# Kernel optimization log

Measured on AMD Instinct MI355X. Metric: run time of the kernel, lower is better.

## Reference

```python
import jax, jax.numpy as jnp
import numpy as np

HIDDEN = 64
ALPHA = 0.2  # leaky relu negative slope
NEG_INF = -9e15


def setup_inputs() -> dict:
    key = jax.random.key(0)
    k1, k2, k3, k4, k5 = jax.random.split(key, 5)
    b, N, Fin, Fout = 8, 2048, 512, 256
    inp = jax.random.normal(k1, (b, N, Fin), dtype=jnp.float32)
    adj = jax.random.randint(k2, (b, N, N), 0, 2, dtype=jnp.int32)
    # xavier_uniform with gain=1.414 ~ uniform(-lim, lim)
    def xavier(k, shape):
        lim = 1.414 * np.sqrt(6.0 / (shape[0] + shape[1]))
        return jax.random.uniform(k, shape, jnp.float32, -lim, lim)
    weight = xavier(k3, (Fin, Fout))
    ht = xavier(k4, (Fout, HIDDEN))
    a = xavier(k5, (2 * HIDDEN, 1))
    return {"input": inp, "adj": adj, "weight": weight, "ht": ht, "a": a}


def reference(input, adj, weight, ht, a):
    # h: [b, N, Fout]
    h = jnp.matmul(input, weight)
    # trans_h: [b, N, HIDDEN]
    trans_h = jnp.einsum('bnc,ck->bnk', h, ht)
    # The original cat([th_i, th_j]) @ a decomposes as th_i@a1 + th_j@a2
    a1, a2 = a[:HIDDEN, 0], a[HIDDEN:, 0]
    f1 = trans_h @ a1  # [b, N] source (row) term
    f2 = trans_h @ a2  # [b, N] target (col) term
    e = f1[:, :, None] + f2[:, None, :]  # [b, N, N]
    e = jnp.where(e >= 0, e, ALPHA * e)  # leaky relu
    scores = jnp.where(adj > 0, e, NEG_INF)
    attention = jax.nn.softmax(scores, axis=2)
    # dropout is identity in eval mode (deterministic reference)
    h_prime = jnp.matmul(attention, h)  # [b, N, Fout]
    return jax.nn.elu(h_prime)  # concat=True
```

## Files before the change

kernel.cpp:

```cpp
#include <hip/hip_runtime.h>

typedef float f32x4 __attribute__((ext_vector_type(4)));
typedef short s16x8 __attribute__((ext_vector_type(8)));

#define NN 2048
#define FIN 512
#define FOUT 256
#define L2E 1.4426950408889634f

__device__ __forceinline__ unsigned short f2bf(float f) {
  unsigned u = __builtin_bit_cast(unsigned, f);
  u += 0x7fffu + ((u >> 16) & 1u);
  return (unsigned short)(u >> 16);
}

__device__ __forceinline__ unsigned pkbf(float lo, float hi) {
  unsigned r;
  asm("v_cvt_pk_bf16_f32 %0, %1, %2" : "=v"(r) : "v"(lo), "v"(hi));
  return r;
}

__device__ __forceinline__ float exp2a(float x) {
  float r;
  asm("v_exp_f32 %0, %1" : "=v"(r) : "v"(x));
  return r;
}

__global__ __launch_bounds__(256) void prep_vecs_k(const float* __restrict__ W,
                                                   const float* __restrict__ HT,
                                                   const float* __restrict__ A,
                                                   float* __restrict__ v1,
                                                   float* __restrict__ v2) {
  __shared__ __align__(16) float w1[256];
  __shared__ __align__(16) float w2[256];
  int t = threadIdx.x;
  {
    float s1 = 0.f, s2 = 0.f;
    for (int k = 0; k < 64; k++) {
      float h = HT[t * 64 + k];
      s1 += h * A[k];
      s2 += h * A[64 + k];
    }
    w1[t] = s1;
    w2[t] = s2;
  }
  __syncthreads();
  int wv = t >> 6, l = t & 63;
  int c = blockIdx.x * 4 + wv;
  float4 u1 = *(const float4*)(w1 + l * 4);
  float4 u2 = *(const float4*)(w2 + l * 4);
  float4 x = *(const float4*)(W + (size_t)c * FOUT + l * 4);
  float a1 = x.x * u1.x + x.y * u1.y + x.z * u1.z + x.w * u1.w;
  float a2 = x.x * u2.x + x.y * u2.y + x.z * u2.z + x.w * u2.w;
  for (int o = 32; o; o >>= 1) {
    a1 += __shfl_xor(a1, o);
    a2 += __shfl_xor(a2, o);
  }
  if (l == 0) {
    v1[c] = a1;
    v2[c] = a2;
  }
}

__global__ void prep_wT_k(const float* __restrict__ W, unsigned short* __restrict__ wT) {
  int id = blockIdx.x * 256 + threadIdx.x;
  int f = id >> 9, c = id & 511;
  wT[id] = f2bf(W[c * FOUT + f]);
}

__global__ __launch_bounds__(512) void compress_k(const int* __restrict__ adj,
                                                  unsigned* __restrict__ bits) {
  int ct = blockIdx.x * 512 + threadIdx.x;
  const int4* src = (const int4*)adj + (size_t)ct * 16;
  unsigned w0 = 0u, w1 = 0u;
#pragma unroll
  for (int k = 0; k < 8; k++) {
    int4 a = src[k];
    unsigned nib = (unsigned)(a.x > 0) | ((unsigned)(a.y > 0) << 1) |
                   ((unsigned)(a.z > 0) << 2) | ((unsigned)(a.w > 0) << 3);
    w0 |= nib << (k * 4);
  }
#pragma unroll
  for (int k = 0; k < 8; k++) {
    int4 a = src[8 + k];
    unsigned nib = (unsigned)(a.x > 0) | ((unsigned)(a.y > 0) << 1) |
                   ((unsigned)(a.z > 0) << 2) | ((unsigned)(a.w > 0) << 3);
    w1 |= nib << (k * 4);
  }
  uint2 o;
  o.x = w0;
  o.y = w1;
  *(uint2*)(bits + (size_t)ct * 2) = o;
}

__global__ __launch_bounds__(512) void gemm1_k(const float* __restrict__ inp,
                                               const unsigned short* __restrict__ wT,
                                               unsigned short* __restrict__ hT,
                                               const float* __restrict__ v1,
                                               const float* __restrict__ v2,
                                               float* __restrict__ f1,
                                               float* __restrict__ f2) {
  int tid = threadIdx.x;
  int w = tid >> 6, l = tid & 63, lr = l & 15, lg = l >> 4;
  int jtile = blockIdx.x * 64;
  f32x4 acc[2][4] = {};
  float s1[4] = {0.f, 0.f, 0.f, 0.f}, s2[4] = {0.f, 0.f, 0.f, 0.f};
  for (int c0 = 0; c0 < FIN; c0 += 32) {
    s16x8 af[2];
#pragma unroll
    for (int mf = 0; mf < 2; mf++) {
      int f = w * 32 + mf * 16 + lr;
      af[mf] = *(const s16x8*)(wT + (size_t)f * FIN + c0 + lg * 8);
    }
    float4 va0, va1, vb0, vb1;
    if (w == 0) {
      va0 = *(const float4*)(v1 + c0 + lg * 8);
      va1 = *(const float4*)(v1 + c0 + lg * 8 + 4);
      vb0 = *(const float4*)(v2 + c0 + lg * 8);
      vb1 = *(const float4*)(v2 + c0 + lg * 8 + 4);
    }
    s16x8 bfv[4];
#pragma unroll
    for (int nf = 0; nf < 4; nf++) {
      int jg = jtile + nf * 16 + lr;
      const float* p = inp + (size_t)jg * FIN + c0 + lg * 8;
      float4 x0 = *(const float4*)p;
      float4 x1 = *(const float4*)(p + 4);
      s16x8 t;
      t[0] = (short)f2bf(x0.x); t[1] = (short)f2bf(x0.y);
      t[2] = (short)f2bf(x0.z); t[3] = (short)f2bf(x0.w);
      t[4] = (short)f2bf(x1.x); t[5] = (short)f2bf(x1.y);
      t[6] = (short)f2bf(x1.z); t[7] = (short)f2bf(x1.w);
      bfv[nf] = t;
      if (w == 0) {
        s1[nf] += x0.x * va0.x + x0.y * va0.y + x0.z * va0.z + x0.w * va0.w +
                  x1.x * va1.x + x1.y * va1.y + x1.z * va1.z + x1.w * va1.w;
        s2[nf] += x0.x * vb0.x + x0.y * vb0.y + x0.z * vb0.z + x0.w * vb0.w +
                  x1.x * vb1.x + x1.y * vb1.y + x1.z * vb1.z + x1.w * vb1.w;
      }
    }
#pragma unroll
    for (int mf = 0; mf < 2; mf++)
#pragma unroll
      for (int nf = 0; nf < 4; nf++)
        acc[mf][nf] =
            __builtin_amdgcn_mfma_f32_16x16x32_bf16(af[mf], bfv[nf], acc[mf][nf], 0, 0, 0);
  }
  int bb = jtile >> 11, jl = jtile & 2047;
#pragma unroll
  for (int mf = 0; mf < 2; mf++)
#pragma unroll
    for (int nf = 0; nf < 4; nf++)
#pragma unroll
      for (int r = 0; r < 4; r++) {
        int f = w * 32 + mf * 16 + lg * 4 + r;
        int j = jl + nf * 16 + lr;
        hT[((size_t)bb * FOUT + f) * (size_t)NN + j] = f2bf(acc[mf][nf][r]);
      }
  if (w == 0) {
#pragma unroll
    for (int nf = 0; nf < 4; nf++) {
      float a = s1[nf], b = s2[nf];
      a += __shfl_xor(a, 16); a += __shfl_xor(a, 32);
      b += __shfl_xor(b, 16); b += __shfl_xor(b, 32);
      if (lg == 0) {
        int jg = jtile + nf * 16 + lr;
        f1[jg] = a * L2E;
        f2[jg] = b * L2E;
      }
    }
  }
}

__global__ __launch_bounds__(256, 2) void pv_k(const unsigned* __restrict__ bits,
                                               const unsigned short* __restrict__ hT,
                                               const float* __restrict__ f1,
                                               const float* __restrict__ f2,
                                               float* __restrict__ out) {
  int tid = threadIdx.x;
  int w = tid >> 6;
  int l = tid & 63, lr = l & 15, lg = l >> 4;
  int blk = blockIdx.x;
  int b = blk >> 6;
  int i0 = (blk & 63) * 32;
  int f0 = w * 64;
  int ja = lg * 8;

  const unsigned* brow0 = bits + ((size_t)(b * NN + i0 + lr)) * 64;
  const unsigned* brow1 = brow0 + 16 * 64;
  const unsigned short* hp_base = hT + ((size_t)b * FOUT + f0 + lr) * NN + ja;
  const float* f2b = f2 + b * NN + ja;
  float fi0 = f1[b * NN + i0 + lr];
  float fi1 = f1[b * NN + i0 + 16 + lr];
  unsigned sh = (unsigned)(lg * 8);

  f32x4 acc[2][4] = {};
  float ls0 = 0.f, ls1 = 0.f;

  auto pcompb = [&](float fi, unsigned byt, const float4& fA, const float4& fB,
                    float& ls) -> s16x8 {
    float e0 = fi + fA.x, e1 = fi + fA.y, e2 = fi + fA.z, e3 = fi + fA.w;
    float e4 = fi + fB.x, e5 = fi + fB.y, e6 = fi + fB.z, e7 = fi + fB.w;
    e0 = fmaxf(e0, 0.2f * e0); e1 = fmaxf(e1, 0.2f * e1);
    e2 = fmaxf(e2, 0.2f * e2); e3 = fmaxf(e3, 0.2f * e3);
    e4 = fmaxf(e4, 0.2f * e4); e5 = fmaxf(e5, 0.2f * e5);
    e6 = fmaxf(e6, 0.2f * e6); e7 = fmaxf(e7, 0.2f * e7);
    float p0 = (byt & 1u)   ? exp2a(e0) : 0.f;
    float p1 = (byt & 2u)   ? exp2a(e1) : 0.f;
    float p2 = (byt & 4u)   ? exp2a(e2) : 0.f;
    float p3 = (byt & 8u)   ? exp2a(e3) : 0.f;
    float p4 = (byt & 16u)  ? exp2a(e4) : 0.f;
    float p5 = (byt & 32u)  ? exp2a(e5) : 0.f;
    float p6 = (byt & 64u)  ? exp2a(e6) : 0.f;
    float p7 = (byt & 128u) ? exp2a(e7) : 0.f;
    ls += ((p0 + p1) + (p2 + p3)) + ((p4 + p5) + (p6 + p7));
    union { unsigned u[4]; s16x8 v; } pk;
    pk.u[0] = pkbf(p0, p1); pk.u[1] = pkbf(p2, p3);
    pk.u[2] = pkbf(p4, p5); pk.u[3] = pkbf(p6, p7);
    return pk.v;
  };

  s16x8 pb0 = *(const s16x8*)(hp_base);
  s16x8 pb1 = *(const s16x8*)(hp_base + 16 * NN);
  s16x8 pb2 = *(const s16x8*)(hp_base + 32 * NN);
  s16x8 pb3 = *(const s16x8*)(hp_base + 48 * NN);
  float4 pfA = *(const float4*)(f2b);
  float4 pfB = *(const float4*)(f2b + 4);
  uint4 q0 = *(const uint4*)(brow0);
  uint4 q1 = *(const uint4*)(brow1);

  for (int jb = 0; jb < NN; jb += 128) {
    uint4 c0 = q0, c1 = q1;
    if (jb + 128 < NN) {
      q0 = *(const uint4*)(brow0 + (jb >> 5) + 4);
      q1 = *(const uint4*)(brow1 + (jb >> 5) + 4);
    }
#pragma unroll
    for (int s = 0; s < 4; s++) {
      int j0 = jb + s * 32;
      unsigned wd0 = (s == 0) ? c0.x : (s == 1) ? c0.y : (s == 2) ? c0.z : c0.w;
      unsigned wd1 = (s == 0) ? c1.x : (s == 1) ? c1.y : (s == 2) ? c1.z : c1.w;
      s16x8 cb0 = pb0, cb1 = pb1, cb2 = pb2, cb3 = pb3;
      float4 cfA = pfA, cfB = pfB;
      if (j0 + 32 < NN) {
        const unsigned short* hp = hp_base + j0 + 32;
        pb0 = *(const s16x8*)(hp);
        pb1 = *(const s16x8*)(hp + 16 * NN);
        pb2 = *(const s16x8*)(hp + 32 * NN);
        pb3 = *(const s16x8*)(hp + 48 * NN);
        pfA = *(const float4*)(f2b + j0 + 32);
        pfB = *(const float4*)(f2b + j0 + 36);
      }
      s16x8 af0 = pcompb(fi0, (wd0 >> sh) & 0xffu, cfA, cfB, ls0);
      s16x8 af1 = pcompb(fi1, (wd1 >> sh) & 0xffu, cfA, cfB, ls1);
      acc[0][0] = __builtin_amdgcn_mfma_f32_16x16x32_bf16(af0, cb0, acc[0][0], 0, 0, 0);
      acc[0][1] = __builtin_amdgcn_mfma_f32_16x16x32_bf16(af0, cb1, acc[0][1], 0, 0, 0);
      acc[0][2] = __builtin_amdgcn_mfma_f32_16x16x32_bf16(af0, cb2, acc[0][2], 0, 0, 0);
      acc[0][3] = __builtin_amdgcn_mfma_f32_16x16x32_bf16(af0, cb3, acc[0][3], 0, 0, 0);
      acc[1][0] = __builtin_amdgcn_mfma_f32_16x16x32_bf16(af1, cb0, acc[1][0], 0, 0, 0);
      acc[1][1] = __builtin_amdgcn_mfma_f32_16x16x32_bf16(af1, cb1, acc[1][1], 0, 0, 0);
      acc[1][2] = __builtin_amdgcn_mfma_f32_16x16x32_bf16(af1, cb2, acc[1][2], 0, 0, 0);
      acc[1][3] = __builtin_amdgcn_mfma_f32_16x16x32_bf16(af1, cb3, acc[1][3], 0, 0, 0);
    }
  }

  ls0 += __shfl_xor(ls0, 16); ls0 += __shfl_xor(ls0, 32);
  ls1 += __shfl_xor(ls1, 16); ls1 += __shfl_xor(ls1, 32);
  float rd0[4], rd1[4];
#pragma unroll
  for (int r = 0; r < 4; r++) {
    rd0[r] = 1.0f / __shfl(ls0, lg * 4 + r);
    rd1[r] = 1.0f / __shfl(ls1, lg * 4 + r);
  }

#pragma unroll
  for (int nf = 0; nf < 4; nf++)
#pragma unroll
    for (int r = 0; r < 4; r++) {
      int m0 = lg * 4 + r;
      int fcol = f0 + nf * 16 + lr;
      float v0 = acc[0][nf][r] * rd0[r];
      v0 = (v0 > 0.f) ? v0 : expm1f(v0);
      out[((size_t)(b * NN + i0 + m0)) * FOUT + fcol] = v0;
      float v1_ = acc[1][nf][r] * rd1[r];
      v1_ = (v1_ > 0.f) ? v1_ : expm1f(v1_);
      out[((size_t)(b * NN + i0 + 16 + m0)) * FOUT + fcol] = v1_;
    }
}

extern "C" void kernel_launch(void* const* d_in, const int* in_sizes, int n_in,
                              void* d_out, int out_size, void* d_ws, size_t ws_size,
                              hipStream_t stream) {
  const float* inp = (const float*)d_in[0];
  const int* adj   = (const int*)d_in[1];
  const float* W   = (const float*)d_in[2];
  const float* HT  = (const float*)d_in[3];
  const float* A   = (const float*)d_in[4];
  float* out = (float*)d_out;

  char* ws = (char*)d_ws;
  float* v1 = (float*)ws;
  float* v2 = v1 + 512;
  float* f1 = (float*)(ws + 4096);
  float* f2 = (float*)(ws + 69632);
  unsigned short* wT = (unsigned short*)(ws + 135168);
  unsigned short* hT = (unsigned short*)(ws + 397312);
  unsigned* bits = (unsigned*)(ws + 8785920);

  hipLaunchKernelGGL(prep_vecs_k, dim3(128), dim3(256), 0, stream, W, HT, A, v1, v2);
  hipLaunchKernelGGL(prep_wT_k, dim3(512), dim3(256), 0, stream, W, wT);
  hipLaunchKernelGGL(compress_k, dim3(1024), dim3(512), 0, stream, adj, bits);
  hipLaunchKernelGGL(gemm1_k, dim3(256), dim3(512), 0, stream, inp, wT, hT, v1, v2, f1,
                     f2);
  hipLaunchKernelGGL(pv_k, dim3(512), dim3(256), 0, stream, bits, hT, f1, f2, out);
}
```

Measured before the change: 172.0 us.

## Halve pv_k row tile, double grid, compute softmax row sums via MFMA

The attention-PV kernel now handles 16 rows per block instead of 32, doubling the grid to 1024 blocks and raising launch bounds to 4 blocks per CU to improve occupancy. Softmax denominators now come from an extra MFMA against a vector of bf16 ones instead of scalar adds and cross-lane shuffles. Each block reloads the hT and f2 tiles for half as many rows, so global/L2 traffic for the value matrix doubles. The row sums are now computed from bf16-rounded probabilities, which shifts numerics slightly.

```diff
diff --git a/kernel.cpp b/kernel.cpp
--- a/kernel.cpp
+++ b/kernel.cpp
@@ -172,7 +172,7 @@
   }
 }
 
-__global__ __launch_bounds__(256, 2) void pv_k(const unsigned* __restrict__ bits,
+__global__ __launch_bounds__(256, 4) void pv_k(const unsigned* __restrict__ bits,
                                                const unsigned short* __restrict__ hT,
                                                const float* __restrict__ f1,
                                                const float* __restrict__ f2,
@@ -181,24 +181,23 @@
   int w = tid >> 6;
   int l = tid & 63, lr = l & 15, lg = l >> 4;
   int blk = blockIdx.x;
-  int b = blk >> 6;
-  int i0 = (blk & 63) * 32;
+  int b = blk >> 7;
+  int i0 = (blk & 127) * 16;
   int f0 = w * 64;
   int ja = lg * 8;
 
-  const unsigned* brow0 = bits + ((size_t)(b * NN + i0 + lr)) * 64;
-  const unsigned* brow1 = brow0 + 16 * 64;
+  const unsigned* brow = bits + ((size_t)(b * NN + i0 + lr)) * 64;
   const unsigned short* hp_base = hT + ((size_t)b * FOUT + f0 + lr) * NN + ja;
   const float* f2b = f2 + b * NN + ja;
-  float fi0 = f1[b * NN + i0 + lr];
-  float fi1 = f1[b * NN + i0 + 16 + lr];
+  float fi = f1[b * NN + i0 + lr];
   unsigned sh = (unsigned)(lg * 8);
 
-  f32x4 acc[2][4] = {};
-  float ls0 = 0.f, ls1 = 0.f;
-
-  auto pcompb = [&](float fi, unsigned byt, const float4& fA, const float4& fB,
-                    float& ls) -> s16x8 {
+  f32x4 acc0 = {}, acc1 = {}, acc2 = {}, acc3 = {}, accs = {};
+  s16x8 ones;
+#pragma unroll
+  for (int e = 0; e < 8; e++) ones[e] = (short)0x3F80;
+
+  auto pcompb = [&](unsigned byt, const float4& fA, const float4& fB) -> s16x8 {
     float e0 = fi + fA.x, e1 = fi + fA.y, e2 = fi + fA.z, e3 = fi + fA.w;
     float e4 = fi + fB.x, e5 = fi + fB.y, e6 = fi + fB.z, e7 = fi + fB.w;
     e0 = fmaxf(e0, 0.2f * e0); e1 = fmaxf(e1, 0.2f * e1);
@@ -213,7 +212,6 @@
     float p5 = (byt & 32u)  ? exp2a(e5) : 0.f;
     float p6 = (byt & 64u)  ? exp2a(e6) : 0.f;
     float p7 = (byt & 128u) ? exp2a(e7) : 0.f;
-    ls += ((p0 + p1) + (p2 + p3)) + ((p4 + p5) + (p6 + p7));
     union { unsigned u[4]; s16x8 v; } pk;
     pk.u[0] = pkbf(p0, p1); pk.u[1] = pkbf(p2, p3);
     pk.u[2] = pkbf(p4, p5); pk.u[3] = pkbf(p6, p7);
@@ -226,20 +224,15 @@
   s16x8 pb3 = *(const s16x8*)(hp_base + 48 * NN);
   float4 pfA = *(const float4*)(f2b);
   float4 pfB = *(const float4*)(f2b + 4);
-  uint4 q0 = *(const uint4*)(brow0);
-  uint4 q1 = *(const uint4*)(brow1);
+  uint4 q = *(const uint4*)(brow);
 
   for (int jb = 0; jb < NN; jb += 128) {
-    uint4 c0 = q0, c1 = q1;
-    if (jb + 128 < NN) {
-      q0 = *(const uint4*)(brow0 + (jb >> 5) + 4);
-      q1 = *(const uint4*)(brow1 + (jb >> 5) + 4);
-    }
+    uint4 c = q;
+    if (jb + 128 < NN) q = *(const uint4*)(brow + (jb >> 5) + 4);
 #pragma unroll
     for (int s = 0; s < 4; s++) {
       int j0 = jb + s * 32;
-      unsigned wd0 = (s == 0) ? c0.x : (s == 1) ? c0.y : (s == 2) ? c0.z : c0.w;
-      unsigned wd1 = (s == 0) ? c1.x : (s == 1) ? c1.y : (s == 2) ? c1.z : c1.w;
+      unsigned wd = (s == 0) ? c.x : (s == 1) ? c.y : (s == 2) ? c.z : c.w;
       s16x8 cb0 = pb0, cb1 = pb1, cb2 = pb2, cb3 = pb3;
       float4 cfA = pfA, cfB = pfB;
       if (j0 + 32 < NN) {
@@ -251,41 +244,28 @@
         pfA = *(const float4*)(f2b + j0 + 32);
         pfB = *(const float4*)(f2b + j0 + 36);
       }
-      s16x8 af0 = pcompb(fi0, (wd0 >> sh) & 0xffu, cfA, cfB, ls0);
-      s16x8 af1 = pcompb(fi1, (wd1 >> sh) & 0xffu, cfA, cfB, ls1);
-      acc[0][0] = __builtin_amdgcn_mfma_f32_16x16x32_bf16(af0, cb0, acc[0][0], 0, 0, 0);
-      acc[0][1] = __builtin_amdgcn_mfma_f32_16x16x32_bf16(af0, cb1, acc[0][1], 0, 0, 0);
-      acc[0][2] = __builtin_amdgcn_mfma_f32_16x16x32_bf16(af0, cb2, acc[0][2], 0, 0, 0);
-      acc[0][3] = __builtin_amdgcn_mfma_f32_16x16x32_bf16(af0, cb3, acc[0][3], 0, 0, 0);
-      acc[1][0] = __builtin_amdgcn_mfma_f32_16x16x32_bf16(af1, cb0, acc[1][0], 0, 0, 0);
-      acc[1][1] = __builtin_amdgcn_mfma_f32_16x16x32_bf16(af1, cb1, acc[1][1], 0, 0, 0);
-      acc[1][2] = __builtin_amdgcn_mfma_f32_16x16x32_bf16(af1, cb2, acc[1][2], 0, 0, 0);
-      acc[1][3] = __builtin_amdgcn_mfma_f32_16x16x32_bf16(af1, cb3, acc[1][3], 0, 0, 0);
-    }
-  }
-
-  ls0 += __shfl_xor(ls0, 16); ls0 += __shfl_xor(ls0, 32);
-  ls1 += __shfl_xor(ls1, 16); ls1 += __shfl_xor(ls1, 32);
-  float rd0[4], rd1[4];
-#pragma unroll
-  for (int r = 0; r < 4; r++) {
-    rd0[r] = 1.0f / __shfl(ls0, lg * 4 + r);
-    rd1[r] = 1.0f / __shfl(ls1, lg * 4 + r);
-  }
-
-#pragma unroll
-  for (int nf = 0; nf < 4; nf++)
+      s16x8 af = pcompb((wd >> sh) & 0xffu, cfA, cfB);
+      acc0 = __builtin_amdgcn_mfma_f32_16x16x32_bf16(af, cb0, acc0, 0, 0, 0);
+      acc1 = __builtin_amdgcn_mfma_f32_16x16x32_bf16(af, cb1, acc1, 0, 0, 0);
+      acc2 = __builtin_amdgcn_mfma_f32_16x16x32_bf16(af, cb2, acc2, 0, 0, 0);
+      acc3 = __builtin_amdgcn_mfma_f32_16x16x32_bf16(af, cb3, acc3, 0, 0, 0);
+      accs = __builtin_amdgcn_mfma_f32_16x16x32_bf16(af, ones, accs, 0, 0, 0);
+    }
+  }
+
+  float rd[4];
+#pragma unroll
+  for (int r = 0; r < 4; r++) rd[r] = 1.0f / accs[r];
+
+  auto wr = [&](const f32x4& a, int nf) {
 #pragma unroll
     for (int r = 0; r < 4; r++) {
-      int m0 = lg * 4 + r;
-      int fcol = f0 + nf * 16 + lr;
-      float v0 = acc[0][nf][r] * rd0[r];
-      v0 = (v0 > 0.f) ? v0 : expm1f(v0);
-      out[((size_t)(b * NN + i0 + m0)) * FOUT + fcol] = v0;
-      float v1_ = acc[1][nf][r] * rd1[r];
-      v1_ = (v1_ > 0.f) ? v1_ : expm1f(v1_);
-      out[((size_t)(b * NN + i0 + 16 + m0)) * FOUT + fcol] = v1_;
-    }
+      float v = a[r] * rd[r];
+      v = (v > 0.f) ? v : expm1f(v);
+      out[((size_t)(b * NN + i0 + lg * 4 + r)) * FOUT + f0 + nf * 16 + lr] = v;
+    }
+  };
+  wr(acc0, 0); wr(acc1, 1); wr(acc2, 2); wr(acc3, 3);
 }
 
 extern "C" void kernel_launch(void* const* d_in, const int* in_sizes, int n_in,
@@ -312,5 +292,5 @@
   hipLaunchKernelGGL(compress_k, dim3(1024), dim3(512), 0, stream, adj, bits);
   hipLaunchKernelGGL(gemm1_k, dim3(256), dim3(512), 0, stream, inp, wT, hT, v1, v2, f1,
                      f2);
-  hipLaunchKernelGGL(pv_k, dim3(512), dim3(256), 0, stream, bits, hT, f1, f2, out);
-}
+  hipLaunchKernelGGL(pv_k, dim3(1024), dim3(256), 0, stream, bits, hT, f1, f2, out);
+}
```

Result: slower. 229.7 us (+33.5%).
